# Optimization experiments

Hardware: AMD Instinct MI355X
Metric: run time of the kernel (lower is better)

The kernel has to match this reference:

```python
import jax, jax.numpy as jnp
import numpy as np

NUM_CLUSTERS = 50000
LN_EPS = 1e-5


def setup_inputs() -> dict:
    key = jax.random.key(0)
    ks = jax.random.split(key, 8)
    N, E, H = 1000000, 64, 64
    x = jax.random.normal(ks[0], (N, E), dtype=jnp.float32)
    cluster = jax.random.randint(ks[1], (N,), 0, NUM_CLUSTERS, dtype=jnp.int64)
    batch = jax.random.randint(ks[2], (N,), 0, 64, dtype=jnp.int64)
    W1 = jax.random.normal(ks[3], (E, H), dtype=jnp.float32) / np.sqrt(E)
    b1 = jnp.zeros((H,), dtype=jnp.float32)
    ln_g = jnp.ones((H,), dtype=jnp.float32)
    ln_b = jnp.zeros((H,), dtype=jnp.float32)
    W2 = jax.random.normal(ks[4], (H, E // 2), dtype=jnp.float32) / np.sqrt(H)
    b2 = jnp.zeros((E // 2,), dtype=jnp.float32)
    return {"x": x, "cluster": cluster, "batch": batch, "W1": W1, "b1": b1,
            "ln_g": ln_g, "ln_b": ln_b, "W2": W2, "b2": b2}


def _mlp(x, W1, b1, ln_g, ln_b, W2, b2):
    h = x @ W1 + b1                                   # [N, H]
    mu = jnp.mean(h, axis=-1, keepdims=True)
    var = jnp.mean(jnp.square(h - mu), axis=-1, keepdims=True)
    h = (h - mu) * jax.lax.rsqrt(var + LN_EPS) * ln_g + ln_b
    h = h * jax.nn.sigmoid(h)                         # SiLU
    return h @ W2 + b2                                # [N, E//2]


def reference(x, cluster, batch, W1, b1, ln_g, ln_b, W2, b2):
    out = _mlp(x, W1, b1, ln_g, ln_b, W2, b2)         # [N, E//2]
    cl = cluster.astype(jnp.int32)
    # max-pool per cluster (segment max), then gather back per node
    aggr = jax.ops.segment_max(out, cl, num_segments=NUM_CLUSTERS)  # [C, E//2]
    return jnp.concatenate([out, aggr[cl]], axis=-1)  # [N, E]
```

## Files before the change

kernel.cpp:

```cpp
#include <hip/hip_runtime.h>

#define NUM_CLUSTERS 50000

typedef __attribute__((ext_vector_type(8))) short bfx8;
typedef __attribute__((ext_vector_type(4))) float f32x4;

__device__ __forceinline__ unsigned fkey(float f) {
    unsigned b = __float_as_uint(f);
    return b ^ ((b & 0x80000000u) ? 0xFFFFFFFFu : 0x80000000u);
}
__device__ __forceinline__ float funkey(unsigned k) {
    unsigned b = (k & 0x80000000u) ? (k ^ 0x80000000u) : ~k;
    return __uint_as_float(b);
}
__device__ __forceinline__ unsigned short f2bf(float f) {
    unsigned u = __float_as_uint(f);
    return (unsigned short)((u + 0x7FFFu + ((u >> 16) & 1u)) >> 16);
}

__global__ __launch_bounds__(256) void prep_weights(
    const float* __restrict__ W1, const float* __restrict__ W2,
    unsigned short* __restrict__ w1f, unsigned short* __restrict__ w2f)
{
    int tid = blockIdx.x * 256 + threadIdx.x;
    if (tid < 512) {
        int frag = tid >> 6, lane = tid & 63;
        int ct = frag >> 1, kb = frag & 1;
        int col = ct * 16 + (lane & 15);
        int k0 = kb * 32 + (lane >> 4) * 8;
        #pragma unroll
        for (int i = 0; i < 8; ++i)
            w1f[(frag * 64 + lane) * 8 + i] = f2bf(W1[(k0 + i) * 64 + col]);
    } else if (tid < 768) {
        int frag = (tid - 512) >> 6, lane = tid & 63;
        int ct = frag >> 1, kb = frag & 1;
        int col = ct * 16 + (lane & 15);
        int k0 = kb * 32 + (lane >> 4) * 8;
        #pragma unroll
        for (int i = 0; i < 8; ++i)
            w2f[(frag * 64 + lane) * 8 + i] = f2bf(W2[(k0 + i) * 32 + col]);
    }
}

__global__ __launch_bounds__(256, 5) void mlp_segmax_kernel(
    const float* __restrict__ x, const int* __restrict__ cluster,
    const unsigned short* __restrict__ w1f, const float* __restrict__ b1,
    const float* __restrict__ ln_g, const float* __restrict__ ln_b,
    const unsigned short* __restrict__ w2f, const float* __restrict__ b2,
    float* __restrict__ out, unsigned* __restrict__ aggr, int N)
{
    __shared__ char smem[256 * 128];
    const int t = threadIdx.x;
    const int lane = t & 63;
    const int w = t >> 6;
    const int l15 = lane & 15;
    const int q = lane >> 4;
    const long long wbase = (long long)blockIdx.x * 256 + w * 64;
    if (wbase >= N) return;
    char* wmem = smem + w * 8192;

    #pragma unroll 4
    for (int p = 0; p < 16; ++p) {
        int le = (p * 64 + lane) * 4;
        float4 v = *(const float4*)(x + wbase * 64 + le);
        int row = le >> 6;
        int k = le & 63;
        int g = k >> 3;
        int half = (k >> 2) & 1;
        int phys = row * 128 + ((g ^ (row & 7)) << 4) + (half << 3);
        ushort4 b;
        b.x = f2bf(v.x); b.y = f2bf(v.y); b.z = f2bf(v.z); b.w = f2bf(v.w);
        *(ushort4*)(wmem + phys) = b;
    }

    bfx8 W1F[4][2], W2F[2][2];
    #pragma unroll
    for (int ct = 0; ct < 4; ++ct)
        #pragma unroll
        for (int kb = 0; kb < 2; ++kb)
            W1F[ct][kb] = *(const bfx8*)(w1f + ((ct * 2 + kb) * 64 + lane) * 8);
    #pragma unroll
    for (int ct = 0; ct < 2; ++ct)
        #pragma unroll
        for (int kb = 0; kb < 2; ++kb)
            W2F[ct][kb] = *(const bfx8*)(w2f + ((ct * 2 + kb) * 64 + lane) * 8);

    float g4[4], bb4[4], b1c[4];
    #pragma unroll
    for (int tt = 0; tt < 4; ++tt) {
        g4[tt]  = ln_g[16 * tt + l15];
        bb4[tt] = ln_b[16 * tt + l15];
        b1c[tt] = b1[16 * tt + l15];
    }
    float b2c[2] = { b2[l15], b2[16 + l15] };

    #pragma unroll 1
    for (int g = 0; g < 4; ++g) {
        const int base = g * 16;
        const int arow = base + l15;
        const int arsw = arow & 7;

        bfx8 af[2];
        #pragma unroll
        for (int kb = 0; kb < 2; ++kb)
            af[kb] = *(const bfx8*)(wmem + arow * 128 + (((kb * 4 + q) ^ arsw) << 4));

        f32x4 acc[4];
        #pragma unroll
        for (int tt = 0; tt < 4; ++tt) {
            float b = b1c[tt];
            acc[tt] = (f32x4){b, b, b, b};
        }
        #pragma unroll
        for (int kb = 0; kb < 2; ++kb)
            #pragma unroll
            for (int tt = 0; tt < 4; ++tt)
                acc[tt] = __builtin_amdgcn_mfma_f32_16x16x32_bf16(af[kb], W1F[tt][kb], acc[tt], 0, 0, 0);

        float s[4];
        #pragma unroll
        for (int r = 0; r < 4; ++r)
            s[r] = acc[0][r] + acc[1][r] + acc[2][r] + acc[3][r];
        #pragma unroll
        for (int m = 1; m < 16; m <<= 1)
            #pragma unroll
            for (int r = 0; r < 4; ++r) s[r] += __shfl_xor(s[r], m, 16);
        float mu[4];
        #pragma unroll
        for (int r = 0; r < 4; ++r) mu[r] = s[r] * (1.f / 64.f);
        float vv[4] = {0.f, 0.f, 0.f, 0.f};
        #pragma unroll
        for (int tt = 0; tt < 4; ++tt)
            #pragma unroll
            for (int r = 0; r < 4; ++r) {
                float d = acc[tt][r] - mu[r];
                vv[r] = fmaf(d, d, vv[r]);
            }
        #pragma unroll
        for (int m = 1; m < 16; m <<= 1)
            #pragma unroll
            for (int r = 0; r < 4; ++r) vv[r] += __shfl_xor(vv[r], m, 16);
        float rs[4];
        #pragma unroll
        for (int r = 0; r < 4; ++r) rs[r] = rsqrtf(vv[r] * (1.f / 64.f) + 1e-5f);

        #pragma unroll
        for (int tt = 0; tt < 4; ++tt)
            #pragma unroll
            for (int r = 0; r < 4; ++r) {
                float val = (acc[tt][r] - mu[r]) * rs[r] * g4[tt] + bb4[tt];
                val = val / (1.f + __expf(-val));
                int node = base + q * 4 + r;
                int col = 16 * tt + l15;
                int phys = node * 128 + ((((col >> 3)) ^ (node & 7)) << 4) + ((col & 7) * 2);
                *(unsigned short*)(wmem + phys) = f2bf(val);
            }

        bfx8 hf[2];
        #pragma unroll
        for (int kb = 0; kb < 2; ++kb)
            hf[kb] = *(const bfx8*)(wmem + arow * 128 + (((kb * 4 + q) ^ arsw) << 4));
        f32x4 oacc[2];
        #pragma unroll
        for (int c = 0; c < 2; ++c) {
            float b = b2c[c];
            oacc[c] = (f32x4){b, b, b, b};
        }
        #pragma unroll
        for (int kb = 0; kb < 2; ++kb)
            #pragma unroll
            for (int c = 0; c < 2; ++c)
                oacc[c] = __builtin_amdgcn_mfma_f32_16x16x32_bf16(hf[kb], W2F[c][kb], oacc[c], 0, 0, 0);

        int clr[4];
        #pragma unroll
        for (int r = 0; r < 4; ++r)
            clr[r] = cluster[wbase + base + q * 4 + r];

        unsigned keys[8];
        unsigned* slots[8];
        #pragma unroll
        for (int c = 0; c < 2; ++c)
            #pragma unroll
            for (int r = 0; r < 4; ++r) {
                int i = c * 4 + r;
                float v = oacc[c][r];
                long long node = wbase + base + q * 4 + r;
                out[node * 64 + c * 16 + l15] = v;
                keys[i] = fkey(v);
                slots[i] = aggr + (long long)clr[r] * 32 + c * 16 + l15;
            }
        unsigned olds[8];
        #pragma unroll
        for (int i = 0; i < 8; ++i) olds[i] = *slots[i];
        #pragma unroll
        for (int i = 0; i < 8; ++i)
            if (keys[i] > olds[i]) atomicMax(slots[i], keys[i]);
    }
}

__global__ __launch_bounds__(256) void gather_kernel(
    const int* __restrict__ cluster, const unsigned* __restrict__ aggr,
    float* __restrict__ out, int N)
{
    long long idx = (long long)blockIdx.x * 256 + threadIdx.x;
    if (idx >= (long long)N * 8) return;
    int n = (int)(idx >> 3);
    int k4 = (int)(idx & 7) * 4;
    int c = cluster[n];
    uint4 a = *(const uint4*)(aggr + (size_t)c * 32 + k4);
    float4 o;
    o.x = funkey(a.x); o.y = funkey(a.y); o.z = funkey(a.z); o.w = funkey(a.w);
    *(float4*)(out + (size_t)n * 64 + 32 + k4) = o;
}

extern "C" void kernel_launch(void* const* d_in, const int* in_sizes, int n_in,
                              void* d_out, int out_size, void* d_ws, size_t ws_size,
                              hipStream_t stream) {
    const float* x     = (const float*)d_in[0];
    const int* cluster = (const int*)d_in[1];
    const float* W1    = (const float*)d_in[3];
    const float* b1    = (const float*)d_in[4];
    const float* ln_g  = (const float*)d_in[5];
    const float* ln_b  = (const float*)d_in[6];
    const float* W2    = (const float*)d_in[7];
    const float* b2    = (const float*)d_in[8];
    float* out = (float*)d_out;

    unsigned* aggr = (unsigned*)d_ws;
    unsigned short* w1f = (unsigned short*)((char*)d_ws + (size_t)NUM_CLUSTERS * 32 * 4);
    unsigned short* w2f = w1f + 8 * 64 * 8;

    int N = in_sizes[0] / 64;

    hipMemsetAsync(aggr, 0, (size_t)NUM_CLUSTERS * 32 * sizeof(unsigned), stream);
    prep_weights<<<3, 256, 0, stream>>>(W1, W2, w1f, w2f);

    int blocks1 = (N + 255) / 256;
    mlp_segmax_kernel<<<blocks1, 256, 0, stream>>>(
        x, cluster, w1f, b1, ln_g, ln_b, w2f, b2, out, aggr, N);

    long long total2 = (long long)N * 8;
    int blocks2 = (int)((total2 + 255) / 256);
    gather_kernel<<<blocks2, 256, 0, stream>>>(cluster, aggr, out, N);
}
```

Measured before the change: 293.7 us.

## Stage MLP outputs in LDS for coalesced nontemporal stores; pack bf16 conversion

```diff
diff --git a/kernel.cpp b/kernel.cpp
--- a/kernel.cpp
+++ b/kernel.cpp
@@ -1,4 +1,5 @@
 #include <hip/hip_runtime.h>
+#include <hip/hip_bf16.h>
 
 #define NUM_CLUSTERS 50000
 
@@ -16,6 +17,10 @@
 __device__ __forceinline__ unsigned short f2bf(float f) {
     unsigned u = __float_as_uint(f);
     return (unsigned short)((u + 0x7FFFu + ((u >> 16) & 1u)) >> 16);
+}
+__device__ __forceinline__ unsigned pk2bf(float a, float b) {
+    __hip_bfloat162 h = __float22bfloat162_rn(make_float2(a, b));
+    return *(unsigned*)&h;
 }
 
 __global__ __launch_bounds__(256) void prep_weights(
@@ -68,9 +73,7 @@
         int g = k >> 3;
         int half = (k >> 2) & 1;
         int phys = row * 128 + ((g ^ (row & 7)) << 4) + (half << 3);
-        ushort4 b;
-        b.x = f2bf(v.x); b.y = f2bf(v.y); b.z = f2bf(v.z); b.w = f2bf(v.w);
-        *(ushort4*)(wmem + phys) = b;
+        *(uint2*)(wmem + phys) = make_uint2(pk2bf(v.x, v.y), pk2bf(v.z, v.w));
     }
 
     bfx8 W1F[4][2], W2F[2][2];
@@ -172,11 +175,20 @@
             for (int c = 0; c < 2; ++c)
                 oacc[c] = __builtin_amdgcn_mfma_f32_16x16x32_bf16(hf[kb], W2F[c][kb], oacc[c], 0, 0, 0);
 
+        #pragma unroll
+        for (int c = 0; c < 2; ++c)
+            #pragma unroll
+            for (int r = 0; r < 4; ++r) {
+                int node = base + q * 4 + r;
+                int byte = (c * 16 + l15) * 4;
+                int phys = node * 128 + (((byte >> 4) ^ (node & 7)) << 4) + (byte & 15);
+                *(float*)(wmem + phys) = oacc[c][r];
+            }
+
         int clr[4];
         #pragma unroll
         for (int r = 0; r < 4; ++r)
             clr[r] = cluster[wbase + base + q * 4 + r];
-
         unsigned keys[8];
         unsigned* slots[8];
         #pragma unroll
@@ -184,10 +196,7 @@
             #pragma unroll
             for (int r = 0; r < 4; ++r) {
                 int i = c * 4 + r;
-                float v = oacc[c][r];
-                long long node = wbase + base + q * 4 + r;
-                out[node * 64 + c * 16 + l15] = v;
-                keys[i] = fkey(v);
+                keys[i] = fkey(oacc[c][r]);
                 slots[i] = aggr + (long long)clr[r] * 32 + c * 16 + l15;
             }
         unsigned olds[8];
@@ -196,6 +205,15 @@
         #pragma unroll
         for (int i = 0; i < 8; ++i)
             if (keys[i] > olds[i]) atomicMax(slots[i], keys[i]);
+    }
+
+    #pragma unroll 2
+    for (int p = 0; p < 8; ++p) {
+        int le = (p * 64 + lane) * 4;
+        int row = le >> 5;
+        int c = le & 31;
+        f32x4 v4 = *(const f32x4*)(wmem + row * 128 + (((c >> 2) ^ (row & 7)) << 4));
+        __builtin_nontemporal_store(v4, (f32x4*)(out + (wbase + row) * 64 + c));
     }
 }
 
@@ -209,9 +227,8 @@
     int k4 = (int)(idx & 7) * 4;
     int c = cluster[n];
     uint4 a = *(const uint4*)(aggr + (size_t)c * 32 + k4);
-    float4 o;
-    o.x = funkey(a.x); o.y = funkey(a.y); o.z = funkey(a.z); o.w = funkey(a.w);
-    *(float4*)(out + (size_t)n * 64 + 32 + k4) = o;
+    f32x4 o = {funkey(a.x), funkey(a.y), funkey(a.z), funkey(a.w)};
+    __builtin_nontemporal_store(o, (f32x4*)(out + (size_t)n * 64 + 32 + k4));
 }
 
 extern "C" void kernel_launch(void* const* d_in, const int* in_sizes, int n_in,
```

After: 271.6 us. 7.5% less time.
